# Kernel optimization log

Hardware: AMD Instinct MI355X
Metric: run time of the kernel (lower is better)

Reference implementation:

```python
import jax, jax.numpy as jnp
import numpy as np

IN_DIM = 128
OUT_DIM = 256
N_ETYPES = 4
N_STEPS = 8
B = 128
N_NODES = 256
E = 393216
CONCAT = IN_DIM + OUT_DIM


def _conv1d(x, w, b):
    # x: [B, C, L], w: [O, I, K] -> valid conv, stride 1
    y = jax.lax.conv_general_dilated(x, w, (1,), 'VALID', dimension_numbers=('NCH', 'OIH', 'NCH'))
    return y + b[None, :, None]


def _maxpool1d(x, k, s):
    return jax.lax.reduce_window(x, -jnp.inf, jax.lax.max, (1, 1, k), (1, 1, s), 'VALID')


def setup_inputs():
    key = jax.random.key(0)
    ks = jax.random.split(key, 16)
    Nn = B * N_NODES
    sc = 0.05
    f32 = jnp.float32
    return {
        'features': jax.random.normal(ks[0], (Nn, IN_DIM), f32),
        'src': jax.random.randint(ks[1], (E,), 0, Nn),
        'dst': jax.random.randint(ks[2], (E,), 0, Nn),
        'etype': jax.random.randint(ks[3], (E,), 0, N_ETYPES),
        'W_msg': jax.random.normal(ks[4], (N_ETYPES, OUT_DIM, OUT_DIM), f32) * sc,
        'b_msg': jnp.zeros((N_ETYPES, OUT_DIM), f32),
        'gru_Wi': jax.random.normal(ks[5], (OUT_DIM, 3 * OUT_DIM), f32) * sc,
        'gru_Wh': jax.random.normal(ks[6], (OUT_DIM, 3 * OUT_DIM), f32) * sc,
        'gru_bi': jnp.zeros((3 * OUT_DIM,), f32),
        'gru_bh': jnp.zeros((3 * OUT_DIM,), f32),
        'conv1_w': jax.random.normal(ks[7], (OUT_DIM, OUT_DIM, 3), f32) * sc,
        'conv1_b': jnp.zeros((OUT_DIM,), f32),
        'conv2_w': jax.random.normal(ks[8], (OUT_DIM, OUT_DIM, 1), f32) * sc,
        'conv2_b': jnp.zeros((OUT_DIM,), f32),
        'convc1_w': jax.random.normal(ks[9], (CONCAT, CONCAT, 3), f32) * sc,
        'convc1_b': jnp.zeros((CONCAT,), f32),
        'convc2_w': jax.random.normal(ks[10], (CONCAT, CONCAT, 1), f32) * sc,
        'convc2_b': jnp.zeros((CONCAT,), f32),
        'wy': jax.random.normal(ks[11], (OUT_DIM, 1), f32) * sc,
        'by': jnp.zeros((1,), f32),
        'wz': jax.random.normal(ks[12], (CONCAT, 1), f32) * sc,
        'bz': jnp.zeros((1,), f32),
        'num_graphs': B,
    }


def reference(features, src, dst, etype, W_msg, b_msg, gru_Wi, gru_Wh, gru_bi, gru_bh,
              conv1_w, conv1_b, conv2_w, conv2_b, convc1_w, convc1_b, convc2_w, convc2_b,
              wy, by, wz, bz, num_graphs):
    Nn = features.shape[0]
    # DGL GatedGraphConv: pad input feats up to out_feats
    h = jnp.pad(features, ((0, 0), (0, OUT_DIM - IN_DIM)))
    for _ in range(N_STEPS):
        # per-etype linear transform of all nodes: [Nn, T, O]
        H_all = jnp.einsum('nd,tdo->nto', h, W_msg) + b_msg[None]
        msg = H_all[src, etype]                              # [E, O]
        a = jax.ops.segment_sum(msg, dst, num_segments=Nn)   # [Nn, O]
        gi = a @ gru_Wi + gru_bi
        gh = h @ gru_Wh + gru_bh
        ir, iz, ig = jnp.split(gi, 3, axis=-1)
        hr, hz, hg = jnp.split(gh, 3, axis=-1)
        r = jax.nn.sigmoid(ir + hr)
        z = jax.nn.sigmoid(iz + hz)
        g = jnp.tanh(ig + r * hg)
        h = (1.0 - z) * g + z * h
    x_i = features.reshape(num_graphs, -1, IN_DIM)
    h_i = h.reshape(num_graphs, -1, OUT_DIM)
    c_i = jnp.concatenate([h_i, x_i], axis=-1)
    Y1 = _maxpool1d(jax.nn.relu(_conv1d(h_i.transpose(0, 2, 1), conv1_w, conv1_b)), 3, 2)
    Y2 = _maxpool1d(jax.nn.relu(_conv1d(Y1, conv2_w, conv2_b)), 2, 2).transpose(0, 2, 1)
    Z1 = _maxpool1d(jax.nn.relu(_conv1d(c_i.transpose(0, 2, 1), convc1_w, convc1_b)), 3, 2)
    Z2 = _maxpool1d(jax.nn.relu(_conv1d(Z1, convc2_w, convc2_b)), 2, 2).transpose(0, 2, 1)
    before_avg = (Y2 @ wy + by) * (Z2 @ wz + bz)   # [B, L, 1]
    avg = before_avg.mean(axis=1)                    # [B, 1]
    return jax.nn.sigmoid(avg).squeeze(-1)           # [B]
```

## Files before the change

kernel.cpp:

```cpp
#include <hip/hip_runtime.h>

#define DEV static __device__ __forceinline__

typedef float f32x4 __attribute__((ext_vector_type(4)));
typedef __bf16 bf16x8 __attribute__((ext_vector_type(8)));
typedef unsigned int u32x4 __attribute__((ext_vector_type(4)));
typedef unsigned int u32x2 __attribute__((ext_vector_type(2)));

#define NNODE 32768
#define NEDGE 393216
#define EPAD (NEDGE + 16 * NNODE)

DEV unsigned short f2bf(float f) {
    unsigned int u = __builtin_bit_cast(unsigned int, f);
    u += 0x7FFFu + ((u >> 16) & 1u);
    return (unsigned short)(u >> 16);
}
DEV float bf2f(unsigned int b) {
    unsigned int u = b << 16;
    return __builtin_bit_cast(float, u);
}
DEV unsigned int pk2(float a, float b) {
    return (unsigned int)f2bf(a) | ((unsigned int)f2bf(b) << 16);
}
DEV float sigf(float x) { return 1.f / (1.f + __expf(-x)); }

DEV void gld16(const void* g, void* l) {
    __builtin_amdgcn_global_load_lds(
        (const __attribute__((address_space(1))) void*)(g),
        (__attribute__((address_space(3))) void*)(l),
        16, 0, 0);
}


__global__ __launch_bounds__(256) void init_k(
    const float* __restrict__ feat,
    unsigned short* __restrict__ hb0, unsigned short* __restrict__ hb1,
    unsigned short* __restrict__ fb)
{
    int idx = blockIdx.x * 256 + threadIdx.x;
    int r = idx >> 8, c = idx & 255;
    float f = 0.f;
    if (r < NNODE && c < 128) f = feat[(size_t)r * 128 + c];
    unsigned short v = f2bf(f);
    hb0[(size_t)r * 256 + c] = v;
    hb1[(size_t)r * 256 + c] = v;
    if (c < 128) fb[(size_t)r * 128 + c] = v;
}

__global__ __launch_bounds__(256) void prep_all_k(
    const float* __restrict__ Wm,
    const float* __restrict__ Wi, const float* __restrict__ Wh,
    const float* __restrict__ bi, const float* __restrict__ bh,
    const float* __restrict__ c1w, const float* __restrict__ c2w,
    const float* __restrict__ cc1w, const float* __restrict__ cc2w,
    unsigned short* __restrict__ WT, unsigned short* __restrict__ B2T,
    float* __restrict__ b2,
    unsigned short* __restrict__ BTY, unsigned short* __restrict__ BT2,
    unsigned short* __restrict__ BTZ, unsigned short* __restrict__ BTc2)
{
    int gid = blockIdx.x * 256 + threadIdx.x;
    if (gid < 262144) {
        int idx = gid;
        int j = idx >> 8, d = idx & 255;
        int t = j >> 8, o = j & 255;
        WT[idx] = f2bf(Wm[t * 65536 + d * 256 + o]);
    } else if (gid < 786432) {
        int idx = gid - 262144;
        int j = idx >> 9, k = idx & 511;
        int band = j >> 6, g = (j >> 4) & 3, ch = (band << 4) + (j & 15);
        float v = 0.f;
        if (g == 0) v = (k < 256) ? Wi[k * 768 + ch] : Wh[(k - 256) * 768 + ch];
        else if (g == 1) v = (k < 256) ? Wi[k * 768 + 256 + ch] : Wh[(k - 256) * 768 + 256 + ch];
        else if (g == 2) { if (k < 256) v = Wi[k * 768 + 512 + ch]; }
        else { if (k >= 256) v = Wh[(k - 256) * 768 + 512 + ch]; }
        B2T[idx] = f2bf(v);
    } else if (gid < 787456) {
        int j = gid - 786432;
        int band = j >> 6, g = (j >> 4) & 3, ch = (band << 4) + (j & 15);
        float v;
        if (g == 0) v = bi[ch] + bh[ch];
        else if (g == 1) v = bi[256 + ch] + bh[256 + ch];
        else if (g == 2) v = bi[512 + ch];
        else v = bh[512 + ch];
        b2[j] = v;
    } else {
        int idx = gid - 787456;
        if (idx < 196608) {
            int o = idx / 768, kk = idx - o * 768, k = kk >> 8, c = kk & 255;
            BTY[idx] = f2bf(c1w[o * 768 + c * 3 + k]);
        } else if (idx < 262144) {
            int r = idx - 196608, o = r >> 8, c = r & 255;
            BT2[r] = f2bf(c2w[o * 256 + c]);
        } else if (idx < 704512) {
            int jx = idx - 262144, o = jx / 1152, kk = jx - o * 1152;
            float v;
            if (kk < 768) { int k = kk >> 8, c = kk & 255; v = cc1w[o * 1152 + c * 3 + k]; }
            else { int r = kk - 768, kf = r >> 7, cf = r & 127; v = cc1w[o * 1152 + (256 + cf) * 3 + kf]; }
            BTZ[jx] = f2bf(v);
        } else {
            int r = idx - 704512, o = r / 384, c = r - o * 384;
            BTc2[r] = f2bf(cc2w[o * 384 + c]);
        }
    }
}


__global__ __launch_bounds__(256) void pc_k(
    const int* __restrict__ dst, int* __restrict__ cnt, int* __restrict__ edat)
{
    int e = blockIdx.x * 256 + threadIdx.x;
    edat[e] = NNODE;
    if (e < NEDGE) atomicAdd(&cnt[dst[e]], 1);
}

__global__ __launch_bounds__(1024) void scan1_k(
    const int* __restrict__ cnt, int* __restrict__ rp, int* __restrict__ bsum)
{
    __shared__ int buf[1024];
    int b = blockIdx.x, tid = threadIdx.x;
    int n = (b << 10) + tid;
    int v = (cnt[n] + 15) & ~15;
    buf[tid] = v;
    __syncthreads();
    for (int off = 1; off < 1024; off <<= 1) {
        int x = (tid >= off) ? buf[tid - off] : 0;
        __syncthreads();
        buf[tid] += x;
        __syncthreads();
    }
    rp[n] = buf[tid] - v;
    if (tid == 1023) bsum[b] = buf[1023];
}

__global__ __launch_bounds__(64) void scan2_k(
    const int* __restrict__ bsum, int* __restrict__ boff, int* __restrict__ rp)
{
    int lane = threadIdx.x;
    int v = (lane < 32) ? bsum[lane] : 0;
    int s = v;
    #pragma unroll
    for (int off = 1; off < 32; off <<= 1) {
        int x = __shfl_up(s, off, 64);
        if (lane >= off) s += x;
    }
    if (lane < 32) boff[lane] = s - v;
    if (lane == 32) boff[32] = 0;
    if (lane == 31) rp[NNODE] = s;
}

__global__ __launch_bounds__(256) void fill_k(
    const int* __restrict__ src, const int* __restrict__ dst,
    const int* __restrict__ et, const int* __restrict__ rp,
    const int* __restrict__ boff,
    int* __restrict__ pos, int* __restrict__ edat)
{
    int e = blockIdx.x * 256 + threadIdx.x;
    int d = dst[e];
    int p = atomicAdd(&pos[d], 1);
    edat[rp[d] + boff[d >> 10] + p] = src[e] | (et[e] << 20);
}


__global__ __launch_bounds__(256) void agg2_k(
    const int* __restrict__ rp, const int* __restrict__ boff,
    const int* __restrict__ edat,
    const unsigned short* __restrict__ Hmsg, unsigned short* __restrict__ Aonly)
{
    int wave = threadIdx.x >> 6, lane = threadIdx.x & 63;
    int n = (blockIdx.x << 2) + wave;
    int e0 = rp[n] + boff[n >> 10];
    int e1 = rp[n + 1] + boff[(n + 1) >> 10];
    int half = lane >> 5, lc = lane & 31;
    float a0 = 0.f, a1 = 0.f, a2 = 0.f, a3 = 0.f;
    float a4 = 0.f, a5 = 0.f, a6 = 0.f, a7 = 0.f;
    const unsigned short* hc = Hmsg + (lc << 3);
    for (int e = e0; e < e1; e += 16) {
        u32x4 v[8];
        #pragma unroll
        for (int q = 0; q < 8; q++) {
            int d = edat[e + (q << 1) + half];
            v[q] = *(const u32x4*)(hc + ((size_t)(d & 0xFFFFF) << 10) + ((d >> 20) << 8));
        }
        #pragma unroll
        for (int q = 0; q < 8; q++) {
            a0 += bf2f(v[q].x & 0xFFFFu); a1 += bf2f(v[q].x >> 16);
            a2 += bf2f(v[q].y & 0xFFFFu); a3 += bf2f(v[q].y >> 16);
            a4 += bf2f(v[q].z & 0xFFFFu); a5 += bf2f(v[q].z >> 16);
            a6 += bf2f(v[q].w & 0xFFFFu); a7 += bf2f(v[q].w >> 16);
        }
    }
    a0 += __shfl_xor(a0, 32, 64); a1 += __shfl_xor(a1, 32, 64);
    a2 += __shfl_xor(a2, 32, 64); a3 += __shfl_xor(a3, 32, 64);
    a4 += __shfl_xor(a4, 32, 64); a5 += __shfl_xor(a5, 32, 64);
    a6 += __shfl_xor(a6, 32, 64); a7 += __shfl_xor(a7, 32, 64);
    if (half == 0) {
        u32x4 p;
        p.x = pk2(a0, a1); p.y = pk2(a2, a3);
        p.z = pk2(a4, a5); p.w = pk2(a6, a7);
        *(u32x4*)(Aonly + (size_t)n * 256 + (lc << 3)) = p;
    }
}

#define STAGE_COORDS                                            \
    int srow[4], scb[4], soff[4];                               \
    _Pragma("unroll")                                           \
    for (int p = 0; p < 4; p++) {                               \
        int c = wave + p * 4;                                   \
        int half = c >> 3, cc = c & 7;                          \
        srow[p] = cc * 16 + (lane >> 2);                        \
        scb[p] = (((lane & 3) ^ ((lane >> 3) & 3)) + half * 4) * 8; \
        soff[p] = half * 4096 + cc * 512;                       \
    }

#define MFMA64(AS, BS)                                                        \
    _Pragma("unroll")                                                         \
    for (int h = 0; h < 2; h++) {                                             \
        bf16x8 af[4], bfr[4];                                                 \
        _Pragma("unroll")                                                     \
        for (int i = 0; i < 4; i++)                                           \
            af[i] = *(const bf16x8*)(&(AS)[h * 4096 + (qm + i * 16 + fm) * 32 + fksw * 8]); \
        _Pragma("unroll")                                                     \
        for (int i = 0; i < 4; i++)                                           \
            bfr[i] = *(const bf16x8*)(&(BS)[h * 4096 + (qn + i * 16 + fm) * 32 + fksw * 8]); \
        _Pragma("unroll")                                                     \
        for (int i = 0; i < 4; i++)                                           \
            _Pragma("unroll")                                                 \
            for (int j = 0; j < 4; j++)                                       \
                acc[i][j] = __builtin_amdgcn_mfma_f32_16x16x32_bf16(bfr[j], af[i], acc[i][j], 0, 0, 0); \
    }

#define MFMA64G(AS, BS, SK)                                                   \
    _Pragma("unroll")                                                         \
    for (int h = 0; h < 2; h++) {                                             \
        bf16x8 af[4], bfr[4];                                                 \
        _Pragma("unroll")                                                     \
        for (int i = 0; i < 4; i++)                                           \
            af[i] = *(const bf16x8*)(&(AS)[h * 4096 + (qm + i * 16 + fm) * 32 + fksw * 8]); \
        _Pragma("unroll")                                                     \
        for (int j = 0; j < 4; j++) {                                         \
            if (j == (SK)) continue;                                          \
            bfr[j] = *(const bf16x8*)(&(BS)[h * 4096 + (qn + j * 16 + fm) * 32 + fksw * 8]); \
        }                                                                     \
        _Pragma("unroll")                                                     \
        for (int i = 0; i < 4; i++)                                           \
            _Pragma("unroll")                                                 \
            for (int j = 0; j < 4; j++) {                                     \
                if (j == (SK)) continue;                                      \
                acc[i][j] = __builtin_amdgcn_mfma_f32_16x16x32_bf16(bfr[j], af[i], acc[i][j], 0, 0, 0); \
            }                                                                 \
    }

template<int NT>
__global__ __launch_bounds__(256) void gemm_hmsg(
    const unsigned short* __restrict__ A,
    const unsigned short* __restrict__ Bt,
    unsigned short* __restrict__ Cb,
    const float* __restrict__ bias)
{
    __shared__ __align__(16) unsigned short As0[128 * 64];
    __shared__ __align__(16) unsigned short As1[128 * 64];
    __shared__ __align__(16) unsigned short Bs0[128 * 64];
    __shared__ __align__(16) unsigned short Bs1[128 * 64];
    const int tid = threadIdx.x;
    int id = blockIdx.x;
    { int per = gridDim.x >> 3; id = (id & 7) * per + (id >> 3); }
    const int bm = id >> 3, bn = id & 7;
    const int wave = tid >> 6, lane = tid & 63;
    const unsigned short* Ag = A + (size_t)(bm * 128) * 256;
    const unsigned short* Bg = Bt + (size_t)(bn * 128) * 256;
    const int qm = (wave & 1) << 6, qn = (wave >> 1) << 6;
    const int fm = lane & 15, fkv = lane >> 4;
    const int fksw = fkv ^ ((fm >> 1) & 3);
    STAGE_COORDS

    auto stageA = [&](int kb, unsigned short* dst) {
        #pragma unroll
        for (int p = 0; p < 4; p++)
            gld16(Ag + (size_t)srow[p] * 256 + kb + scb[p], dst + soff[p]);
    };
    auto stageB = [&](int kb, unsigned short* dst) {
        #pragma unroll
        for (int p = 0; p < 4; p++)
            gld16(Bg + (size_t)srow[p] * 256 + kb + scb[p], dst + soff[p]);
    };

    f32x4 acc[4][4] = {};

    stageA(0, As0); stageB(0, Bs0);
    __syncthreads();
    unsigned short *Ac = As0, *An = As1, *Bc = Bs0, *Bn = Bs1;
    #pragma unroll
    for (int kb = 0; kb < NT * 64; kb += 64) {
        if (kb + 64 < NT * 64) { stageA(kb + 64, An); stageB(kb + 64, Bn); }
        MFMA64(Ac, Bc)
        __syncthreads();
        { auto t = Ac; Ac = An; An = t; }
        { auto t = Bc; Bc = Bn; Bn = t; }
    }

    const int m0 = bm * 128 + qm + fm;
    const int n0 = bn * 128 + qn + (fkv << 2);
    #pragma unroll
    for (int i = 0; i < 4; i++) {
        int row = m0 + i * 16;
        #pragma unroll
        for (int j = 0; j < 4; j++) {
            int col = n0 + j * 16;
            float4 bv = *(const float4*)(bias + col);
            u32x2 p;
            p.x = pk2(acc[i][j][0] + bv.x, acc[i][j][1] + bv.y);
            p.y = pk2(acc[i][j][2] + bv.z, acc[i][j][3] + bv.w);
            *(u32x2*)(Cb + (size_t)row * 1024 + col) = p;
        }
    }
}

__global__ __launch_bounds__(256) void gemm_bt(
    const unsigned short* __restrict__ A, int lda,
    const unsigned short* __restrict__ Bt,
    unsigned short* __restrict__ Cb, int ldcb,
    const float* __restrict__ bias,
    int N, int K, int swz, int relu)
{
    __shared__ __align__(16) unsigned short As0[128 * 64];
    __shared__ __align__(16) unsigned short As1[128 * 64];
    __shared__ __align__(16) unsigned short Bs0[128 * 64];
    __shared__ __align__(16) unsigned short Bs1[128 * 64];
    const int tid = threadIdx.x;
    int id = blockIdx.x;
    if (swz) { int per = gridDim.x >> 3; id = (id & 7) * per + (id >> 3); }
    const int nb = N >> 7;
    const int bm = id / nb, bn = id - bm * nb;
    const int wave = tid >> 6, lane = tid & 63;
    const unsigned short* Ag = A + (size_t)(bm * 128) * lda;
    const unsigned short* Bg = Bt + (size_t)(bn * 128) * K;
    const int qm = (wave & 1) << 6, qn = (wave >> 1) << 6;
    const int fm = lane & 15, fkv = lane >> 4;
    const int fksw = fkv ^ ((fm >> 1) & 3);
    STAGE_COORDS

    auto stageA = [&](int kb, unsigned short* dst) {
        #pragma unroll
        for (int p = 0; p < 4; p++)
            gld16(Ag + (size_t)srow[p] * lda + kb + scb[p], dst + soff[p]);
    };
    auto stageB = [&](int kb, unsigned short* dst) {
        #pragma unroll
        for (int p = 0; p < 4; p++)
            gld16(Bg + (size_t)srow[p] * K + kb + scb[p], dst + soff[p]);
    };

    f32x4 acc[4][4] = {};

    stageA(0, As0); stageB(0, Bs0);
    __syncthreads();
    unsigned short *Ac = As0, *An = As1, *Bc = Bs0, *Bn = Bs1;
    for (int kb = 0; kb < K; kb += 64) {
        if (kb + 64 < K) { stageA(kb + 64, An); stageB(kb + 64, Bn); }
        MFMA64(Ac, Bc)
        __syncthreads();
        { auto t = Ac; Ac = An; An = t; }
        { auto t = Bc; Bc = Bn; Bn = t; }
    }

    const int m0 = bm * 128 + qm + fm;
    const int n0 = bn * 128 + qn + (fkv << 2);
    #pragma unroll
    for (int i = 0; i < 4; i++) {
        int row = m0 + i * 16;
        #pragma unroll
        for (int j = 0; j < 4; j++) {
            int col = n0 + j * 16;
            float v0 = acc[i][j][0], v1 = acc[i][j][1],
                  v2 = acc[i][j][2], v3 = acc[i][j][3];
            if (bias) {
                float4 bv = *(const float4*)(bias + col);
                v0 += bv.x; v1 += bv.y; v2 += bv.z; v3 += bv.w;
            }
            if (relu) {
                v0 = fmaxf(v0, 0.f); v1 = fmaxf(v1, 0.f);
                v2 = fmaxf(v2, 0.f); v3 = fmaxf(v3, 0.f);
            }
            u32x2 p; p.x = pk2(v0, v1); p.y = pk2(v2, v3);
            *(u32x2*)(Cb + (size_t)row * ldcb + col) = p;
        }
    }
}

__global__ __launch_bounds__(256) void gemm_conv(
    const unsigned short* __restrict__ Ah,
    const unsigned short* __restrict__ Af,
    const unsigned short* __restrict__ Bt,
    unsigned short* __restrict__ Cb, int ldcb,
    const float* __restrict__ bias,
    int N, int K)
{
    __shared__ __align__(16) unsigned short As0[128 * 64];
    __shared__ __align__(16) unsigned short As1[128 * 64];
    __shared__ __align__(16) unsigned short Bs0[128 * 64];
    __shared__ __align__(16) unsigned short Bs1[128 * 64];
    const int tid = threadIdx.x;
    int id = blockIdx.x;
    { int per = gridDim.x >> 3; id = (id & 7) * per + (id >> 3); }
    const int nb = N >> 7;
    const int bm = id / nb, bn = id - bm * nb;
    const int wave = tid >> 6, lane = tid & 63;
    const unsigned short* Bg = Bt + (size_t)(bn * 128) * K;
    const int qm = (wave & 1) << 6, qn = (wave >> 1) << 6;
    const int fm = lane & 15, fkv = lane >> 4;
    const int fksw = fkv ^ ((fm >> 1) & 3);
    STAGE_COORDS

    auto stageA = [&](int kb, unsigned short* dst) {
        const unsigned short* base; int ldA, col, shift;
        if (kb < 768) { base = Ah; ldA = 256; shift = kb >> 8; col = kb & 255; }
        else { int r = kb - 768; base = Af; ldA = 128; shift = r >> 7; col = r & 127; }
        const unsigned short* Ag = base + (size_t)(bm * 128 + shift) * ldA + col;
        #pragma unroll
        for (int p = 0; p < 4; p++)
            gld16(Ag + (size_t)srow[p] * ldA + scb[p], dst + soff[p]);
    };
    auto stageB = [&](int kb, unsigned short* dst) {
        #pragma unroll
        for (int p = 0; p < 4; p++)
            gld16(Bg + (size_t)srow[p] * K + kb + scb[p], dst + soff[p]);
    };

    f32x4 acc[4][4] = {};

    stageA(0, As0); stageB(0, Bs0);
    __syncthreads();
    unsigned short *Ac = As0, *An = As1, *Bc = Bs0, *Bn = Bs1;
    for (int kb = 0; kb < K; kb += 64) {
        if (kb + 64 < K) { stageA(kb + 64, An); stageB(kb + 64, Bn); }
        MFMA64(Ac, Bc)
        __syncthreads();
        { auto t = Ac; Ac = An; An = t; }
        { auto t = Bc; Bc = Bn; Bn = t; }
    }

    const int m0 = bm * 128 + qm + fm;
    const int n0 = bn * 128 + qn + (fkv << 2);
    #pragma unroll
    for (int i = 0; i < 4; i++) {
        int row = m0 + i * 16;
        #pragma unroll
        for (int j = 0; j < 4; j++) {
            int col = n0 + j * 16;
            float4 bv = *(const float4*)(bias + col);
            float v0 = fmaxf(acc[i][j][0] + bv.x, 0.f);
            float v1 = fmaxf(acc[i][j][1] + bv.y, 0.f);
            float v2 = fmaxf(acc[i][j][2] + bv.z, 0.f);
            float v3 = fmaxf(acc[i][j][3] + bv.w, 0.f);
            u32x2 p; p.x = pk2(v0, v1); p.y = pk2(v2, v3);
            *(u32x2*)(Cb + (size_t)row * ldcb + col) = p;
        }
    }
}

template<int NT>
__global__ __launch_bounds__(256) void gemm_gru(
    const unsigned short* __restrict__ Aonly,
    const unsigned short* __restrict__ hbc,
    const unsigned short* __restrict__ Bt,
    const float* __restrict__ b2p,
    unsigned short* __restrict__ hbn)
{
    __shared__ __align__(16) unsigned short As0[128 * 64];
    __shared__ __align__(16) unsigned short As1[128 * 64];
    __shared__ __align__(16) unsigned short Bs0[128 * 64];
    __shared__ __align__(16) unsigned short Bs1[128 * 64];
    const int tid = threadIdx.x;
    int id = blockIdx.x;
    { int per = gridDim.x >> 3; id = (id & 7) * per + (id >> 3); }
    const int bm = id >> 3;
    const int bn = id & 7;
    const int wave = tid >> 6, lane = tid & 63;
    const unsigned short* Bg = Bt + (size_t)(bn * 128) * 512;
    const int qm = (wave & 1) << 6, qn = (wave >> 1) << 6;
    const int fm = lane & 15, fkv = lane >> 4;
    const int fksw = fkv ^ ((fm >> 1) & 3);
    STAGE_COORDS

    auto stageA = [&](int kb, unsigned short* dst) {
        const unsigned short* base = (kb < 256) ? Aonly : hbc;
        const unsigned short* Ag = base + (size_t)(bm * 128) * 256 + (kb & 255);
        #pragma unroll
        for (int p = 0; p < 4; p++)
            gld16(Ag + (size_t)srow[p] * 256 + scb[p], dst + soff[p]);
    };
    auto stageB = [&](int kb, unsigned short* dst) {
        #pragma unroll
        for (int p = 0; p < 4; p++)
            gld16(Bg + (size_t)srow[p] * 512 + kb + scb[p], dst + soff[p]);
    };

    f32x4 acc[4][4] = {};

    stageA(0, As0); stageB(0, Bs0);
    __syncthreads();
    unsigned short *Ac = As0, *An = As1, *Bc = Bs0, *Bn = Bs1;
    #pragma unroll
    for (int kb = 0; kb < NT * 64; kb += 64) {
        if (kb + 64 < NT * 64) { stageA(kb + 64, An); stageB(kb + 64, Bn); }
        if (kb < 256) { MFMA64G(Ac, Bc, 3) }
        else          { MFMA64G(Ac, Bc, 2) }
        __syncthreads();
        { auto t = Ac; Ac = An; An = t; }
        { auto t = Bc; Bc = Bn; Bn = t; }
    }

    const int band = (bn << 1) + (qn >> 6);
    const int chb = (band << 4) + (fkv << 2);
    const float4 brv = *(const float4*)(b2p + (band << 6) + 0  + (fkv << 2));
    const float4 bzv = *(const float4*)(b2p + (band << 6) + 16 + (fkv << 2));
    const float4 bgv = *(const float4*)(b2p + (band << 6) + 32 + (fkv << 2));
    const float4 bhv = *(const float4*)(b2p + (band << 6) + 48 + (fkv << 2));
    const float br_[4] = {brv.x, brv.y, brv.z, brv.w};
    const float bz_[4] = {bzv.x, bzv.y, bzv.z, bzv.w};
    const float bg_[4] = {bgv.x, bgv.y, bgv.z, bgv.w};
    const float bh_[4] = {bhv.x, bhv.y, bhv.z, bhv.w};
    const int m0 = bm * 128 + qm + fm;
    #pragma unroll
    for (int i = 0; i < 4; i++) {
        int row = m0 + i * 16;
        u32x2 hv = *(const u32x2*)(hbc + (size_t)row * 256 + chb);
        float hp[4] = {bf2f(hv.x & 0xFFFFu), bf2f(hv.x >> 16),
                       bf2f(hv.y & 0xFFFFu), bf2f(hv.y >> 16)};
        float hn[4];
        #pragma unroll
        for (int r = 0; r < 4; r++) {
            float rg = sigf(acc[i][0][r] + br_[r]);
            float zz = sigf(acc[i][1][r] + bz_[r]);
            float pre = acc[i][2][r] + bg_[r] + rg * (acc[i][3][r] + bh_[r]);
            pre = fminf(fmaxf(pre, -15.f), 15.f);
            float t = __expf(2.f * pre);
            float gq = (t - 1.f) / (t + 1.f);
            hn[r] = (1.f - zz) * gq + zz * hp[r];
        }
        u32x2 p; p.x = pk2(hn[0], hn[1]); p.y = pk2(hn[2], hn[3]);
        *(u32x2*)(hbn + (size_t)row * 256 + chb) = p;
    }
}

__global__ __launch_bounds__(256) void pool_k(
    const unsigned short* __restrict__ in, int ldin, int Lb_in, int L_out,
    int win, int C,
    unsigned short* __restrict__ ob, int ldo)
{
    int idx = blockIdx.x * 256 + threadIdx.x;
    int c = idx % C;
    int row = idx / C;
    int b = row / L_out, lp = row - b * L_out;
    const unsigned short* p = in + (size_t)(b * Lb_in + 2 * lp) * ldin + c;
    float m = bf2f(p[0]);
    for (int d = 1; d < win; d++) m = fmaxf(m, bf2f(p[(size_t)d * ldin]));
    ob[(size_t)row * ldo + c] = f2bf(m);
}

__global__ __launch_bounds__(256) void final_k(
    const unsigned short* __restrict__ CY, const unsigned short* __restrict__ CZ,
    const float* __restrict__ wy, const float* __restrict__ by,
    const float* __restrict__ wz, const float* __restrict__ bz,
    float* __restrict__ out)
{
    __shared__ float ws[4];
    int b = blockIdx.x, tid = threadIdx.x;
    int wave = tid >> 6, lane = tid & 63;
    float wyv[4], wzv[6];
    #pragma unroll
    for (int j = 0; j < 4; j++) wyv[j] = wy[lane * 4 + j];
    #pragma unroll
    for (int j = 0; j < 6; j++) wzv[j] = wz[lane * 6 + j];
    const float byv = by[0], bzv = bz[0];
    float acc = 0.f;
    for (int l = wave; l < 63; l += 4) {
        const unsigned short* y0 = CY + (size_t)(b * 126 + 2 * l) * 256 + lane * 4;
        const unsigned short* y1 = y0 + 256;
        u32x2 u0 = *(const u32x2*)y0, u1 = *(const u32x2*)y1;
        float py =
            fmaxf(bf2f(u0.x & 0xFFFFu), bf2f(u1.x & 0xFFFFu)) * wyv[0] +
            fmaxf(bf2f(u0.x >> 16),     bf2f(u1.x >> 16))     * wyv[1] +
            fmaxf(bf2f(u0.y & 0xFFFFu), bf2f(u1.y & 0xFFFFu)) * wyv[2] +
            fmaxf(bf2f(u0.y >> 16),     bf2f(u1.y >> 16))     * wyv[3];
        const unsigned short* z0 = CZ + (size_t)(b * 126 + 2 * l) * 384 + lane * 6;
        const unsigned short* z1 = z0 + 384;
        float pz = 0.f;
        #pragma unroll
        for (int j = 0; j < 6; j++)
            pz += fmaxf(bf2f(z0[j]), bf2f(z1[j])) * wzv[j];
        #pragma unroll
        for (int off = 32; off > 0; off >>= 1) {
            py += __shfl_down(py, off, 64);
            pz += __shfl_down(pz, off, 64);
        }
        if (lane == 0) acc += (py + byv) * (pz + bzv);
    }
    if (lane == 0) ws[wave] = acc;
    __syncthreads();
    if (tid == 0)
        out[b] = sigf((ws[0] + ws[1] + ws[2] + ws[3]) * (1.f / 63.f));
}


extern "C" void kernel_launch(void* const* d_in, const int* in_sizes, int n_in,
                              void* d_out, int out_size, void* d_ws, size_t ws_size,
                              hipStream_t stream)
{
    const float* feat = (const float*)d_in[0];
    const int* src = (const int*)d_in[1];
    const int* dst = (const int*)d_in[2];
    const int* et  = (const int*)d_in[3];
    const float* Wm  = (const float*)d_in[4];
    const float* bm  = (const float*)d_in[5];
    const float* Wi  = (const float*)d_in[6];
    const float* Wh  = (const float*)d_in[7];
    const float* bi  = (const float*)d_in[8];
    const float* bh  = (const float*)d_in[9];
    const float* c1w = (const float*)d_in[10];
    const float* c1b = (const float*)d_in[11];
    const float* c2w = (const float*)d_in[12];
    const float* c2b = (const float*)d_in[13];
    const float* cc1w = (const float*)d_in[14];
    const float* cc1b = (const float*)d_in[15];
    const float* cc2w = (const float*)d_in[16];
    const float* cc2b = (const float*)d_in[17];
    const float* wy = (const float*)d_in[18];
    const float* by = (const float*)d_in[19];
    const float* wz = (const float*)d_in[20];
    const float* bz = (const float*)d_in[21];
    float* out = (float*)d_out;

    char* w = (char*)d_ws;
    size_t off = 0;
    auto alloc = [&](size_t bytes) -> char* {
        char* p = w + off; off += (bytes + 255) & ~(size_t)255; return p;
    };
    unsigned short* hb0 = (unsigned short*)alloc((size_t)(NNODE + 8) * 256 * 2);
    unsigned short* hb1 = (unsigned short*)alloc((size_t)(NNODE + 8) * 256 * 2);
    unsigned short* fb  = (unsigned short*)alloc((size_t)(NNODE + 8) * 128 * 2);
    unsigned short* Aonly = (unsigned short*)alloc((size_t)NNODE * 256 * 2);
    char* R = alloc((size_t)(NNODE + 1) * 1024 * 2);
    unsigned short* Hmsg = (unsigned short*)R;
    unsigned short* CbY  = (unsigned short*)R;
    unsigned short* CbZ  = (unsigned short*)(R + (size_t)NNODE * 256 * 2);
    unsigned short* P    = (unsigned short*)alloc((size_t)16128 * 384 * 2);
    unsigned short* Cb2Y = (unsigned short*)alloc((size_t)16128 * 256 * 2);
    unsigned short* Cb2Z = (unsigned short*)alloc((size_t)16128 * 384 * 2);
    unsigned short* WT   = (unsigned short*)alloc(1024 * 256 * 2);
    unsigned short* B2T  = (unsigned short*)alloc(1024 * 512 * 2);
    float* b2            = (float*)alloc(1024 * 4);
    unsigned short* BTY  = (unsigned short*)alloc(256 * 768 * 2);
    unsigned short* BT2  = (unsigned short*)alloc(256 * 256 * 2);
    unsigned short* BTZ  = (unsigned short*)alloc(384 * 1152 * 2);
    unsigned short* BTc2 = (unsigned short*)alloc(384 * 384 * 2);
    int* rp     = (int*)alloc((NNODE + 1) * 4);
    int* pos    = (int*)alloc(NNODE * 4);
    int* cnt    = (int*)alloc(NNODE * 4);
    int* bsum   = (int*)alloc(32 * 4);
    int* boff   = (int*)alloc(33 * 4);
    int* edat   = (int*)alloc((size_t)EPAD * 4);

    hipLaunchKernelGGL(init_k, dim3(NNODE + 8), dim3(256), 0, stream, feat, hb0, hb1, fb);
    hipLaunchKernelGGL(prep_all_k, dim3(6404), dim3(256), 0, stream,
                       Wm, Wi, Wh, bi, bh, c1w, c2w, cc1w, cc2w,
                       WT, B2T, b2, BTY, BT2, BTZ, BTc2);
    hipMemsetAsync(pos, 0, NNODE * 4, stream);
    hipMemsetAsync(cnt, 0, NNODE * 4, stream);
    hipMemsetAsync(Hmsg + (size_t)NNODE * 1024, 0, 1024 * 2, stream);
    hipLaunchKernelGGL(pc_k, dim3(EPAD / 256), dim3(256), 0, stream, dst, cnt, edat);
    hipLaunchKernelGGL(scan1_k, dim3(32), dim3(1024), 0, stream, cnt, rp, bsum);
    hipLaunchKernelGGL(scan2_k, dim3(1), dim3(64), 0, stream, bsum, boff, rp);
    hipLaunchKernelGGL(fill_k, dim3(NEDGE / 256), dim3(256), 0, stream,
                       src, dst, et, rp, boff, pos, edat);

    unsigned short* hbuf[2] = {hb0, hb1};
    for (int step = 0; step < 8; step++) {
        unsigned short* cur = hbuf[step & 1];
        unsigned short* nxt = hbuf[(step + 1) & 1];
        if (step == 0)
            hipLaunchKernelGGL((gemm_hmsg<2>), dim3(2048), dim3(256), 0, stream,
                cur, WT, Hmsg, bm);
        else
            hipLaunchKernelGGL((gemm_hmsg<4>), dim3(2048), dim3(256), 0, stream,
                cur, WT, Hmsg, bm);
        hipLaunchKernelGGL(agg2_k, dim3(NNODE / 4), dim3(256), 0, stream,
            rp, boff, edat, Hmsg, Aonly);
        if (step == 0)
            hipLaunchKernelGGL((gemm_gru<6>), dim3(2048), dim3(256), 0, stream,
                Aonly, cur, B2T, b2, nxt);
        else
            hipLaunchKernelGGL((gemm_gru<8>), dim3(2048), dim3(256), 0, stream,
                Aonly, cur, B2T, b2, nxt);
    }

    hipLaunchKernelGGL(gemm_conv, dim3(512), dim3(256), 0, stream,
        hb0, (const unsigned short*)nullptr, BTY, CbY, 256, c1b, 256, 768);
    hipLaunchKernelGGL(pool_k, dim3(16128), dim3(256), 0, stream,
        CbY, 256, 256, 126, 3, 256, P, 256);
    hipLaunchKernelGGL(gemm_bt, dim3(252), dim3(256), 0, stream,
        P, 256, BT2, Cb2Y, 256, c2b, 256, 256, 0, 1);

    hipLaunchKernelGGL(gemm_conv, dim3(768), dim3(256), 0, stream,
        hb0, fb, BTZ, CbZ, 384, cc1b, 384, 1152);
    hipLaunchKernelGGL(pool_k, dim3(24192), dim3(256), 0, stream,
        CbZ, 384, 256, 126, 3, 384, P, 384);
    hipLaunchKernelGGL(gemm_bt, dim3(378), dim3(256), 0, stream,
        P, 384, BTc2, Cb2Z, 384, cc2b, 384, 384, 0, 1);

    hipLaunchKernelGGL(final_k, dim3(128), dim3(256), 0, stream,
        Cb2Y, Cb2Z, wy, by, wz, bz, out);
}
```

Measured before the change: 1.139 ms.

## Fuse maxpool into the following 1x1-conv GEMM A-tile load

The separate pool_k kernel and its intermediate buffer P go away. The 1x1 conv GEMM now loads three consecutive conv1 output rows per A row, takes the elementwise bf16 max in registers and writes the pooled tile to LDS. Two memsets are merged into one, and zeroing of the Hmsg pad row moves into init_k. This saves a write and reread of the pooled tensor and two launches, in exchange for register-path A loads instead of async global-to-LDS loads. The max is taken on raw bf16 bit patterns, which is only valid because inputs are post-ReLU and non-negative.

```diff
diff --git a/kernel.cpp b/kernel.cpp
--- a/kernel.cpp
+++ b/kernel.cpp
@@ -6,6 +6,7 @@
 typedef __bf16 bf16x8 __attribute__((ext_vector_type(8)));
 typedef unsigned int u32x4 __attribute__((ext_vector_type(4)));
 typedef unsigned int u32x2 __attribute__((ext_vector_type(2)));
+typedef unsigned short u16x8 __attribute__((ext_vector_type(8)));
 
 #define NNODE 32768
 #define NEDGE 393216
@@ -36,7 +37,7 @@
 __global__ __launch_bounds__(256) void init_k(
     const float* __restrict__ feat,
     unsigned short* __restrict__ hb0, unsigned short* __restrict__ hb1,
-    unsigned short* __restrict__ fb)
+    unsigned short* __restrict__ fb, unsigned short* __restrict__ HmsgZ)
 {
     int idx = blockIdx.x * 256 + threadIdx.x;
     int r = idx >> 8, c = idx & 255;
@@ -46,6 +47,8 @@
     hb0[(size_t)r * 256 + c] = v;
     hb1[(size_t)r * 256 + c] = v;
     if (c < 128) fb[(size_t)r * 128 + c] = v;
+    if (r >= NNODE && r < NNODE + 4)
+        HmsgZ[(size_t)(r - NNODE) * 256 + c] = 0;
 }
 
 __global__ __launch_bounds__(256) void prep_all_k(
@@ -316,78 +319,6 @@
     }
 }
 
-__global__ __launch_bounds__(256) void gemm_bt(
-    const unsigned short* __restrict__ A, int lda,
-    const unsigned short* __restrict__ Bt,
-    unsigned short* __restrict__ Cb, int ldcb,
-    const float* __restrict__ bias,
-    int N, int K, int swz, int relu)
-{
-    __shared__ __align__(16) unsigned short As0[128 * 64];
-    __shared__ __align__(16) unsigned short As1[128 * 64];
-    __shared__ __align__(16) unsigned short Bs0[128 * 64];
-    __shared__ __align__(16) unsigned short Bs1[128 * 64];
-    const int tid = threadIdx.x;
-    int id = blockIdx.x;
-    if (swz) { int per = gridDim.x >> 3; id = (id & 7) * per + (id >> 3); }
-    const int nb = N >> 7;
-    const int bm = id / nb, bn = id - bm * nb;
-    const int wave = tid >> 6, lane = tid & 63;
-    const unsigned short* Ag = A + (size_t)(bm * 128) * lda;
-    const unsigned short* Bg = Bt + (size_t)(bn * 128) * K;
-    const int qm = (wave & 1) << 6, qn = (wave >> 1) << 6;
-    const int fm = lane & 15, fkv = lane >> 4;
-    const int fksw = fkv ^ ((fm >> 1) & 3);
-    STAGE_COORDS
-
-    auto stageA = [&](int kb, unsigned short* dst) {
-        #pragma unroll
-        for (int p = 0; p < 4; p++)
-            gld16(Ag + (size_t)srow[p] * lda + kb + scb[p], dst + soff[p]);
-    };
-    auto stageB = [&](int kb, unsigned short* dst) {
-        #pragma unroll
-        for (int p = 0; p < 4; p++)
-            gld16(Bg + (size_t)srow[p] * K + kb + scb[p], dst + soff[p]);
-    };
-
-    f32x4 acc[4][4] = {};
-
-    stageA(0, As0); stageB(0, Bs0);
-    __syncthreads();
-    unsigned short *Ac = As0, *An = As1, *Bc = Bs0, *Bn = Bs1;
-    for (int kb = 0; kb < K; kb += 64) {
-        if (kb + 64 < K) { stageA(kb + 64, An); stageB(kb + 64, Bn); }
-        MFMA64(Ac, Bc)
-        __syncthreads();
-        { auto t = Ac; Ac = An; An = t; }
-        { auto t = Bc; Bc = Bn; Bn = t; }
-    }
-
-    const int m0 = bm * 128 + qm + fm;
-    const int n0 = bn * 128 + qn + (fkv << 2);
-    #pragma unroll
-    for (int i = 0; i < 4; i++) {
-        int row = m0 + i * 16;
-        #pragma unroll
-        for (int j = 0; j < 4; j++) {
-            int col = n0 + j * 16;
-            float v0 = acc[i][j][0], v1 = acc[i][j][1],
-                  v2 = acc[i][j][2], v3 = acc[i][j][3];
-            if (bias) {
-                float4 bv = *(const float4*)(bias + col);
-                v0 += bv.x; v1 += bv.y; v2 += bv.z; v3 += bv.w;
-            }
-            if (relu) {
-                v0 = fmaxf(v0, 0.f); v1 = fmaxf(v1, 0.f);
-                v2 = fmaxf(v2, 0.f); v3 = fmaxf(v3, 0.f);
-            }
-            u32x2 p; p.x = pk2(v0, v1); p.y = pk2(v2, v3);
-            *(u32x2*)(Cb + (size_t)row * ldcb + col) = p;
-        }
-    }
-}
-
 __global__ __launch_bounds__(256) void gemm_conv(
     const unsigned short* __restrict__ Ah,
     const unsigned short* __restrict__ Af,
@@ -459,6 +390,94 @@
     }
 }
 
+__global__ __launch_bounds__(256) void gemm_bt_pool(
+    const unsigned short* __restrict__ CbX, int ldin,
+    const unsigned short* __restrict__ Bt,
+    unsigned short* __restrict__ Cb, int ldcb,
+    const float* __restrict__ bias,
+    int N, int K)
+{
+    __shared__ __align__(16) unsigned short As0[128 * 64];
+    __shared__ __align__(16) unsigned short As1[128 * 64];
+    __shared__ __align__(16) unsigned short Bs0[128 * 64];
+    __shared__ __align__(16) unsigned short Bs1[128 * 64];
+    const int tid = threadIdx.x;
+    int id = blockIdx.x;
+    const int nb = N >> 7;
+    const int bm = id / nb, bn = id - bm * nb;
+    const int wave = tid >> 6, lane = tid & 63;
+    const unsigned short* Bg = Bt + (size_t)(bn * 128) * K;
+    const int qm = (wave & 1) << 6, qn = (wave >> 1) << 6;
+    const int fm = lane & 15, fkv = lane >> 4;
+    const int fksw = fkv ^ ((fm >> 1) & 3);
+    STAGE_COORDS
+
+    int row0[4];
+    #pragma unroll
+    for (int p = 0; p < 4; p++) {
+        int arow = bm * 128 + srow[p];
+        int b = arow / 126, lp = arow - b * 126;
+        row0[p] = b * 256 + 2 * lp;
+    }
+
+    u16x8 va[4][3];
+    auto loadA3 = [&](int kb) {
+        #pragma unroll
+        for (int p = 0; p < 4; p++) {
+            const unsigned short* s = CbX + (size_t)row0[p] * ldin + kb + scb[p];
+            va[p][0] = *(const u16x8*)s;
+            va[p][1] = *(const u16x8*)(s + ldin);
+            va[p][2] = *(const u16x8*)(s + 2 * ldin);
+        }
+    };
+    auto writeA = [&](unsigned short* dst) {
+        #pragma unroll
+        for (int p = 0; p < 4; p++) {
+            u16x8 m = __builtin_elementwise_max(
+                __builtin_elementwise_max(va[p][0], va[p][1]), va[p][2]);
+            *(u16x8*)(dst + soff[p] + lane * 8) = m;
+        }
+    };
+    auto stageB = [&](int kb, unsigned short* dst) {
+        #pragma unroll
+        for (int p = 0; p < 4; p++)
+            gld16(Bg + (size_t)srow[p] * K + kb + scb[p], dst + soff[p]);
+    };
+
+    f32x4 acc[4][4] = {};
+
+    loadA3(0); writeA(As0); stageB(0, Bs0);
+    __syncthreads();
+    unsigned short *Ac = As0, *An = As1, *Bc = Bs0, *Bn = Bs1;
+    for (int kb = 0; kb < K; kb += 64) {
+        bool more = (kb + 64 < K);
+        if (more) { loadA3(kb + 64); stageB(kb + 64, Bn); }
+        MFMA64(Ac, Bc)
+        if (more) writeA(An);
+        __syncthreads();
+        { auto t = Ac; Ac = An; An = t; }
+        { auto t = Bc; Bc = Bn; Bn = t; }
+    }
+
+    const int m0 = bm * 128 + qm + fm;
+    const int n0 = bn * 128 + qn + (fkv << 2);
+    #pragma unroll
+    for (int i = 0; i < 4; i++) {
+        int row = m0 + i * 16;
+        #pragma unroll
+        for (int j = 0; j < 4; j++) {
+            int col = n0 + j * 16;
+            float4 bv = *(const float4*)(bias + col);
+            float v0 = fmaxf(acc[i][j][0] + bv.x, 0.f);
+            float v1 = fmaxf(acc[i][j][1] + bv.y, 0.f);
+            float v2 = fmaxf(acc[i][j][2] + bv.z, 0.f);
+            float v3 = fmaxf(acc[i][j][3] + bv.w, 0.f);
+            u32x2 p; p.x = pk2(v0, v1); p.y = pk2(v2, v3);
+            *(u32x2*)(Cb + (size_t)row * ldcb + col) = p;
+        }
+    }
+}
+
 template<int NT>
 __global__ __launch_bounds__(256) void gemm_gru(
     const unsigned short* __restrict__ Aonly,
@@ -542,21 +561,6 @@
         u32x2 p; p.x = pk2(hn[0], hn[1]); p.y = pk2(hn[2], hn[3]);
         *(u32x2*)(hbn + (size_t)row * 256 + chb) = p;
     }
-}
-
-__global__ __launch_bounds__(256) void pool_k(
-    const unsigned short* __restrict__ in, int ldin, int Lb_in, int L_out,
-    int win, int C,
-    unsigned short* __restrict__ ob, int ldo)
-{
-    int idx = blockIdx.x * 256 + threadIdx.x;
-    int c = idx % C;
-    int row = idx / C;
-    int b = row / L_out, lp = row - b * L_out;
-    const unsigned short* p = in + (size_t)(b * Lb_in + 2 * lp) * ldin + c;
-    float m = bf2f(p[0]);
-    for (int d = 1; d < win; d++) m = fmaxf(m, bf2f(p[(size_t)d * ldin]));
-    ob[(size_t)row * ldo + c] = f2bf(m);
 }
 
 __global__ __launch_bounds__(256) void final_k(
@@ -645,7 +649,6 @@
     unsigned short* Hmsg = (unsigned short*)R;
     unsigned short* CbY  = (unsigned short*)R;
     unsigned short* CbZ  = (unsigned short*)(R + (size_t)NNODE * 256 * 2);
-    unsigned short* P    = (unsigned short*)alloc((size_t)16128 * 384 * 2);
     unsigned short* Cb2Y = (unsigned short*)alloc((size_t)16128 * 256 * 2);
     unsigned short* Cb2Z = (unsigned short*)alloc((size_t)16128 * 384 * 2);
     unsigned short* WT   = (unsigned short*)alloc(1024 * 256 * 2);
@@ -662,13 +665,12 @@
     int* boff   = (int*)alloc(33 * 4);
     int* edat   = (int*)alloc((size_t)EPAD * 4);
 
-    hipLaunchKernelGGL(init_k, dim3(NNODE + 8), dim3(256), 0, stream, feat, hb0, hb1, fb);
+    hipLaunchKernelGGL(init_k, dim3(NNODE + 8), dim3(256), 0, stream,
+                       feat, hb0, hb1, fb, Hmsg + (size_t)NNODE * 1024);
     hipLaunchKernelGGL(prep_all_k, dim3(6404), dim3(256), 0, stream,
                        Wm, Wi, Wh, bi, bh, c1w, c2w, cc1w, cc2w,
                        WT, B2T, b2, BTY, BT2, BTZ, BTc2);
-    hipMemsetAsync(pos, 0, NNODE * 4, stream);
-    hipMemsetAsync(cnt, 0, NNODE * 4, stream);
-    hipMemsetAsync(Hmsg + (size_t)NNODE * 1024, 0, 1024 * 2, stream);
+    hipMemsetAsync(pos, 0, 2 * NNODE * 4, stream);
     hipLaunchKernelGGL(pc_k, dim3(EPAD / 256), dim3(256), 0, stream, dst, cnt, edat);
     hipLaunchKernelGGL(scan1_k, dim3(32), dim3(1024), 0, stream, cnt, rp, bsum);
     hipLaunchKernelGGL(scan2_k, dim3(1), dim3(64), 0, stream, bsum, boff, rp);
@@ -697,17 +699,13 @@
 
     hipLaunchKernelGGL(gemm_conv, dim3(512), dim3(256), 0, stream,
         hb0, (const unsigned short*)nullptr, BTY, CbY, 256, c1b, 256, 768);
-    hipLaunchKernelGGL(pool_k, dim3(16128), dim3(256), 0, stream,
-        CbY, 256, 256, 126, 3, 256, P, 256);
-    hipLaunchKernelGGL(gemm_bt, dim3(252), dim3(256), 0, stream,
-        P, 256, BT2, Cb2Y, 256, c2b, 256, 256, 0, 1);
+    hipLaunchKernelGGL(gemm_bt_pool, dim3(252), dim3(256), 0, stream,
+        CbY, 256, BT2, Cb2Y, 256, c2b, 256, 256);
 
     hipLaunchKernelGGL(gemm_conv, dim3(768), dim3(256), 0, stream,
         hb0, fb, BTZ, CbZ, 384, cc1b, 384, 1152);
-    hipLaunchKernelGGL(pool_k, dim3(24192), dim3(256), 0, stream,
-        CbZ, 384, 256, 126, 3, 384, P, 384);
-    hipLaunchKernelGGL(gemm_bt, dim3(378), dim3(256), 0, stream,
-        P, 384, BTc2, Cb2Z, 384, cc2b, 384, 384, 0, 1);
+    hipLaunchKernelGGL(gemm_bt_pool, dim3(378), dim3(256), 0, stream,
+        CbZ, 384, BTc2, Cb2Z, 384, cc2b, 384, 384);
 
     hipLaunchKernelGGL(final_k, dim3(128), dim3(256), 0, stream,
         Cb2Y, Cb2Z, wy, by, wz, bz, out);
```

After: 1.118 ms. Within noise of the previous version (-1.8%).
